# Kernel optimization log

Hardware: AMD Instinct MI355X
Metric: run time of the kernel (lower is better)

The kernel has to match this reference:

```python
import jax, jax.numpy as jnp
import numpy as np

N, E, B = 20000, 200000, 16
ND, ED, GD, HD, DOF = 64, 32, 32, 128, 6
PI = 3.14159265358979

def _hat(v):
    x, y, z = v[..., 0], v[..., 1], v[..., 2]
    O = jnp.zeros_like(x)
    return jnp.stack([jnp.stack([O, -z, y], -1),
                      jnp.stack([z, O, -x], -1),
                      jnp.stack([-y, x, O], -1)], -2)

def _so3_exp(phi):
    th2 = jnp.sum(phi * phi, -1, keepdims=True)
    th = jnp.sqrt(th2 + 1e-12)
    a = jnp.where(th < 1e-4, 1.0 - th2 / 6.0, jnp.sin(th) / th)
    b = jnp.where(th < 1e-4, 0.5 - th2 / 24.0, (1.0 - jnp.cos(th)) / th2)
    K = _hat(phi)
    I = jnp.eye(3, dtype=phi.dtype)
    return I + a[..., None] * K + b[..., None] * (K @ K)

def _se3_exp(rho, phi):
    # returns (R, t) of Exp([rho, phi]) with rotation part phi
    th2 = jnp.sum(phi * phi, -1, keepdims=True)
    th = jnp.sqrt(th2 + 1e-12)
    a = jnp.where(th < 1e-4, 1.0 - th2 / 6.0, jnp.sin(th) / th)
    b = jnp.where(th < 1e-4, 0.5 - th2 / 24.0, (1.0 - jnp.cos(th)) / th2)
    c = jnp.where(th < 1e-4, 1.0 / 6.0 - th2 / 120.0, (th - jnp.sin(th)) / (th2 * th))
    K = _hat(phi)
    KK = K @ K
    I = jnp.eye(3, dtype=phi.dtype)
    R = I + a[..., None] * K + b[..., None] * KK
    V = I + b[..., None] * K + c[..., None] * KK
    t = jnp.einsum('nij,nj->ni', V, rho)
    return R, t

def _comp(Ra, ta, Rb, tb):
    return Ra @ Rb, jnp.einsum('nij,nj->ni', Ra, tb) + ta

def _inv(R, t):
    Rt = jnp.swapaxes(R, -1, -2)
    return Rt, -jnp.einsum('nij,nj->ni', Rt, t)

def _vec(R, t):
    # flattened [R | t] 3x4 -> 12
    return jnp.concatenate([R, t[..., None]], -1).reshape(R.shape[0], 12)

def setup_inputs() -> dict:
    key = jax.random.key(0)
    ks = jax.random.split(key, 16)
    T_R = _so3_exp(0.5 * jax.random.normal(ks[0], (N, 3)))
    Tij_R = _so3_exp(0.5 * jax.random.normal(ks[1], (E, 3)))
    return {
        'xfeat': jax.random.normal(ks[2], (N, ND), jnp.float32),
        'T_R': T_R.astype(jnp.float32),
        'T_t': jax.random.normal(ks[3], (N, 3), jnp.float32),
        'edge_feat': jax.random.normal(ks[4], (E, ED), jnp.float32),
        'Tij_R': Tij_R.astype(jnp.float32),
        'Tij_t': jax.random.normal(ks[5], (E, 3), jnp.float32),
        'u': jax.random.normal(ks[6], (B, GD), jnp.float32),
        'edge_index': jax.random.randint(ks[7], (2, E), 0, N),
        'batch': jnp.sort(jax.random.randint(ks[8], (N,), 0, B)),
        'W1': 0.05 * jax.random.normal(ks[9], (2 * ND + 12 + ED, HD), jnp.float32),
        'b1': jnp.zeros((HD,), jnp.float32),
        'W2': 0.05 * jax.random.normal(ks[10], (HD, HD), jnp.float32),
        'b2': jnp.zeros((HD,), jnp.float32),
        'W3': 0.05 * jax.random.normal(ks[11], (HD + GD + ND, HD), jnp.float32),
        'b3': jnp.zeros((HD,), jnp.float32),
        'W4': 0.05 * jax.random.normal(ks[12], (HD, ND + DOF), jnp.float32),
        'b4': jnp.zeros((ND + DOF,), jnp.float32),
    }

def reference(xfeat, T_R, T_t, edge_feat, Tij_R, Tij_t, u,
              edge_index, batch, W1, b1, W2, b2, W3, b3, W4, b4):
    n = xfeat.shape[0]
    i, j = edge_index[0], edge_index[1]
    xfi, xfj = xfeat[i], xfeat[j]
    Ri, ti = T_R[i], T_t[i]
    Rj, tj = T_R[j], T_t[j]
    # T_err_ij = Tj * Ti.inv() * Tij_hat.inv()
    Rii, tii = _inv(Ri, ti)
    Ra, ta = _comp(Rj, tj, Rii, tii)
    Rhi, thi = _inv(Tij_R, Tij_t)
    Reij, teij = _comp(Ra, ta, Rhi, thi)
    # T_err_ji = Ti * Tj.inv() * Tij_hat
    Rji_, tji_ = _inv(Rj, tj)
    Rb, tb = _comp(Ri, ti, Rji_, tji_)
    Reji, teji = _comp(Rb, tb, Tij_R, Tij_t)
    f_ij = jnp.concatenate([xfi, xfj, edge_feat, _vec(Reij, teij)], 1)
    f_ji = jnp.concatenate([xfj, xfi, edge_feat, _vec(Reji, teji)], 1)
    feats = jnp.concatenate([f_ij, f_ji], 0)          # [2E, 172]
    j_both = jnp.concatenate([j, i], 0)               # [2E]
    h = jax.nn.relu(feats @ W1 + b1)
    h = jax.nn.relu(h @ W2 + b2)                      # [2E, HD]
    sums = jax.ops.segment_sum(h, j_both, num_segments=n)
    cnt = jax.ops.segment_sum(jnp.ones((h.shape[0], 1), h.dtype), j_both, num_segments=n)
    aggr = sums / jnp.maximum(cnt, 1.0)               # scatter_mean
    g = jnp.concatenate([aggr, xfeat, u[batch]], 1)
    out = jax.nn.relu(g @ W3 + b3) @ W4 + b4
    xupd, tupd = out[:, :-DOF], out[:, -DOF:]
    rho, phi = tupd[:, :3], tupd[:, 3:]
    # SquashRot: bound rotation angle to pi via tanh
    th = jnp.linalg.norm(phi, axis=-1, keepdims=True)
    phi = phi * (PI * jnp.tanh(th / PI) / (th + 1e-8))
    Rd, td = _se3_exp(rho, phi)
    R_out, t_out = _comp(Rd, td, T_R, T_t)            # boxplus_left: Exp(d) * T
    xfeat_out = xfeat + xupd
    theta = jnp.linalg.norm(phi, axis=-1, keepdims=True)
    return jnp.concatenate([xfeat_out, R_out.reshape(n, 9), t_out, theta], -1)
```

## Files before the change

kernel.cpp:

```cpp
#include <hip/hip_runtime.h>
#include <math.h>

#define ND 64
#define ED 32
#define GD 32
#define HD 128
#define DOF 6
#define K1 172
#define K1PAD 192
#define KG 224
#define N4P 80
#define NOUT 70
#define OUTC 77
#define MT 128
#define HP1 136
#define TDN 16
#define GP 232
#define HP 136
#define OP 84
#define MAXD 96
#define PI_F 3.14159265358979f

typedef short short8 __attribute__((ext_vector_type(8)));
typedef float f32x4  __attribute__((ext_vector_type(4)));

__device__ __forceinline__ unsigned short f2b(float f) {
    unsigned int u = __float_as_uint(f);
    u += 0x7fffu + ((u >> 16) & 1u);
    return (unsigned short)(u >> 16);
}
__device__ __forceinline__ float b2f(unsigned short b) {
    return __uint_as_float(((unsigned int)b) << 16);
}
__device__ __forceinline__ void mul33_abt(const float* A, const float* B, float* C) {
#pragma unroll
    for (int r = 0; r < 3; r++)
#pragma unroll
        for (int c = 0; c < 3; c++)
            C[3*r+c] = A[3*r+0]*B[3*c+0] + A[3*r+1]*B[3*c+1] + A[3*r+2]*B[3*c+2];
}

__global__ void __launch_bounds__(256)
prep(const float* __restrict__ W1, const float* __restrict__ W2,
     const float* __restrict__ W3, const float* __restrict__ W4,
     const float* __restrict__ xfeat, const float* __restrict__ edge_feat,
     unsigned short* __restrict__ W1b, unsigned short* __restrict__ W2b,
     unsigned short* __restrict__ W3b, unsigned short* __restrict__ W4b,
     unsigned short* __restrict__ xb, unsigned short* __restrict__ eb,
     int N, int E)
{
    int idx = blockIdx.x * 256 + threadIdx.x;
    if (idx < K1PAD * HD) {
        int k = idx >> 7, n = idx & 127;
        float v = (k < K1) ? W1[k * HD + n] : 0.f;
        int kc = k >> 5, kr = k & 31, q = kr >> 3, j = kr & 7;
        W1b[(((kc * 8 + (n >> 4)) * 4 + q) * 16 + (n & 15)) * 8 + j] = f2b(v);
        return;
    }
    idx -= K1PAD * HD;
    if (idx < HD * HD) {
        int k = idx >> 7, n = idx & 127;
        int kc = k >> 5, kr = k & 31, q = kr >> 3, j = kr & 7;
        W2b[(((kc * 8 + (n >> 4)) * 4 + q) * 16 + (n & 15)) * 8 + j] = f2b(W2[k * HD + n]);
        return;
    }
    idx -= HD * HD;
    if (idx < KG * HD) {
        int k = idx >> 7, n = idx & 127;
        int sk = (k < HD) ? ((k & 7) * 16 + (k >> 3)) : k;
        int kc = k >> 5, kr = k & 31, q = kr >> 3, j = kr & 7;
        W3b[(((kc * 8 + (n >> 4)) * 4 + q) * 16 + (n & 15)) * 8 + j] = f2b(W3[sk * HD + n]);
        return;
    }
    idx -= KG * HD;
    if (idx < HD * N4P) {
        int k = idx / N4P, n = idx % N4P;
        float v = (n < NOUT) ? W4[k * NOUT + n] : 0.f;
        int kc = k >> 5, kr = k & 31, q = kr >> 3, j = kr & 7;
        W4b[(((kc * 5 + (n >> 4)) * 4 + q) * 16 + (n & 15)) * 8 + j] = f2b(v);
        return;
    }
    idx -= HD * N4P;
    const int nx4 = N * ND / 4;
    if (idx < nx4) {
        const float4 v = *(const float4*)&xfeat[idx * 4];
        ushort4 o; o.x = f2b(v.x); o.y = f2b(v.y); o.z = f2b(v.z); o.w = f2b(v.w);
        *(ushort4*)&xb[idx * 4] = o;
        return;
    }
    idx -= nx4;
    if (idx < E * ED / 4) {
        const float4 v = *(const float4*)&edge_feat[idx * 4];
        ushort4 o; o.x = f2b(v.x); o.y = f2b(v.y); o.z = f2b(v.z); o.w = f2b(v.w);
        *(ushort4*)&eb[idx * 4] = o;
    }
}

__global__ void __launch_bounds__(256)
pose_csr(const float* __restrict__ T_R, const float* __restrict__ T_t,
         const float* __restrict__ Tij_R, const float* __restrict__ Tij_t,
         const int* __restrict__ edge_index,
         unsigned short* __restrict__ poseb, int* __restrict__ cnti,
         int* __restrict__ list, int E)
{
    const int g = blockIdx.x * 256 + threadIdx.x;
    if (g >= 2 * E) return;
    const bool fwd = (g < E);
    const int e = fwd ? g : g - E;
    const int ni = edge_index[e];
    const int nj = edge_index[E + e];
    const int tgt = fwd ? nj : ni;
    const int slot = atomicAdd(&cnti[tgt], 1);
    if (slot < MAXD) list[(size_t)tgt * MAXD + slot] = g;

    float Ri[9], Rj[9], TR[9], ti[3], tj[3], Tt[3];
#pragma unroll
    for (int q = 0; q < 9; q++) { Ri[q] = T_R[9*ni+q]; Rj[q] = T_R[9*nj+q]; TR[q] = Tij_R[9*e+q]; }
#pragma unroll
    for (int q = 0; q < 3; q++) { ti[q] = T_t[3*ni+q]; tj[q] = T_t[3*nj+q]; Tt[q] = Tij_t[3*e+q]; }
    float A[9];
    mul33_abt(Rj, Ri, A);
    float Re[9], te[3];
    if (fwd) {
        mul33_abt(A, TR, Re);
#pragma unroll
        for (int r = 0; r < 3; r++)
            te[r] = tj[r]
                  - (A[3*r+0]*ti[0] + A[3*r+1]*ti[1] + A[3*r+2]*ti[2])
                  - (Re[3*r+0]*Tt[0] + Re[3*r+1]*Tt[1] + Re[3*r+2]*Tt[2]);
    } else {
#pragma unroll
        for (int r = 0; r < 3; r++)
#pragma unroll
            for (int c = 0; c < 3; c++)
                Re[3*r+c] = A[r]*TR[c] + A[3+r]*TR[3+c] + A[6+r]*TR[6+c];
        const float d0 = Tt[0]-tj[0], d1 = Tt[1]-tj[1], d2 = Tt[2]-tj[2];
#pragma unroll
        for (int r = 0; r < 3; r++)
            te[r] = ti[r] + A[r]*d0 + A[3+r]*d1 + A[6+r]*d2;
    }
    short8 p0, p1;
#pragma unroll
    for (int r = 0; r < 2; r++) {
        p0[4*r+0] = (short)f2b(Re[3*r+0]);
        p0[4*r+1] = (short)f2b(Re[3*r+1]);
        p0[4*r+2] = (short)f2b(Re[3*r+2]);
        p0[4*r+3] = (short)f2b(te[r]);
    }
    p1[0] = (short)f2b(Re[6]); p1[1] = (short)f2b(Re[7]);
    p1[2] = (short)f2b(Re[8]); p1[3] = (short)f2b(te[2]);
    p1[4] = 0; p1[5] = 0; p1[6] = 0; p1[7] = 0;
    *(short8*)(poseb + (size_t)g * 16) = p0;
    *(short8*)(poseb + (size_t)g * 16 + 8) = p1;
}

__global__ void __launch_bounds__(256, 3)
edge_kernel(const unsigned short* __restrict__ xb, const unsigned short* __restrict__ eb,
            const unsigned short* __restrict__ poseb, const int* __restrict__ edge_index,
            const unsigned short* __restrict__ W1b, const float* __restrict__ b1,
            const unsigned short* __restrict__ W2b, const float* __restrict__ b2,
            unsigned short* __restrict__ hbuf, int E)
{
    __shared__ unsigned short h1s[4 * 32 * HP1];
    const int tid = threadIdx.x;
    const int wv = tid >> 6, lane = tid & 63;
    const int nl = lane & 15, quad = lane >> 4;
    const int D0 = blockIdx.x * MT + wv * 32;
    const int laneoff = quad * 128 + nl * 8;
    unsigned short* hw = h1s + wv * 32 * HP1;

    int s1[2], s2[2], ee[2], gg[2];
#pragma unroll
    for (int rt = 0; rt < 2; rt++) {
        int g = D0 + rt * 16 + nl;
        if (g >= 2 * E) g = 2 * E - 1;
        const bool fwd = (g < E);
        const int e = fwd ? g : g - E;
        const int ni = edge_index[e];
        const int nj = edge_index[E + e];
        s1[rt] = fwd ? ni : nj;
        s2[rt] = fwd ? nj : ni;
        ee[rt] = e; gg[rt] = g;
    }

    short8 a[2][6];
#pragma unroll
    for (int rt = 0; rt < 2; rt++) {
        a[rt][0] = *(const short8*)(xb + (size_t)s1[rt] * ND + quad * 8);
        a[rt][1] = *(const short8*)(xb + (size_t)s1[rt] * ND + 32 + quad * 8);
        a[rt][2] = *(const short8*)(xb + (size_t)s2[rt] * ND + quad * 8);
        a[rt][3] = *(const short8*)(xb + (size_t)s2[rt] * ND + 32 + quad * 8);
        a[rt][4] = *(const short8*)(eb + (size_t)ee[rt] * ED + quad * 8);
        a[rt][5] = (quad < 2) ? *(const short8*)(poseb + (size_t)gg[rt] * 16 + quad * 8)
                              : (short8)(short)0;
    }

    float bias1[8], bias2[8];
#pragma unroll
    for (int nt = 0; nt < 8; nt++) { bias1[nt] = b1[nt*16 + nl]; bias2[nt] = b2[nt*16 + nl]; }

    f32x4 acc[2][8];
#pragma unroll
    for (int rt = 0; rt < 2; rt++)
#pragma unroll
        for (int nt = 0; nt < 8; nt++) acc[rt][nt] = (f32x4)0.f;

#pragma unroll
    for (int kc = 0; kc < 6; kc++) {
#pragma unroll
        for (int nt = 0; nt < 8; nt++) {
            short8 b = *(const short8*)(W1b + (kc*8 + nt)*512 + laneoff);
            acc[0][nt] = __builtin_amdgcn_mfma_f32_16x16x32_bf16(a[0][kc], b, acc[0][nt], 0, 0, 0);
            acc[1][nt] = __builtin_amdgcn_mfma_f32_16x16x32_bf16(a[1][kc], b, acc[1][nt], 0, 0, 0);
        }
    }

#pragma unroll
    for (int rt = 0; rt < 2; rt++)
#pragma unroll
        for (int nt = 0; nt < 8; nt++) {
            const int col = nt*16 + nl;
#pragma unroll
            for (int r = 0; r < 4; r++)
                hw[(rt*16 + quad*4 + r) * HP1 + col] = f2b(fmaxf(acc[rt][nt][r] + bias1[nt], 0.f));
        }
    asm volatile("s_waitcnt lgkmcnt(0)" ::: "memory");

#pragma unroll
    for (int rt = 0; rt < 2; rt++)
#pragma unroll
        for (int nt = 0; nt < 8; nt++) acc[rt][nt] = (f32x4)0.f;
#pragma unroll
    for (int kc = 0; kc < 4; kc++) {
        short8 a0 = *(const short8*)&hw[( 0 + nl) * HP1 + kc*32 + quad*8];
        short8 a1 = *(const short8*)&hw[(16 + nl) * HP1 + kc*32 + quad*8];
#pragma unroll
        for (int nt = 0; nt < 8; nt++) {
            short8 b = *(const short8*)(W2b + (kc*8 + nt)*512 + laneoff);
            acc[0][nt] = __builtin_amdgcn_mfma_f32_16x16x32_bf16(a0, b, acc[0][nt], 0, 0, 0);
            acc[1][nt] = __builtin_amdgcn_mfma_f32_16x16x32_bf16(a1, b, acc[1][nt], 0, 0, 0);
        }
    }

#pragma unroll
    for (int rt = 0; rt < 2; rt++)
#pragma unroll
        for (int r = 0; r < 4; r++) {
            const int g2 = D0 + rt*16 + quad*4 + r;
            if (g2 < 2 * E) {
                short8 hv;
#pragma unroll
                for (int nt = 0; nt < 8; nt++)
                    hv[nt] = (short)f2b(fmaxf(acc[rt][nt][r] + bias2[nt], 0.f));
                *(short8*)(hbuf + (size_t)g2 * HD + nl*8) = hv;
            }
        }
}

__global__ void __launch_bounds__(256)
node_kernel(const float* __restrict__ xfeat, const float* __restrict__ T_R,
            const float* __restrict__ T_t, const float* __restrict__ u,
            const int* __restrict__ batch,
            const unsigned short* __restrict__ W3b, const float* __restrict__ b3,
            const unsigned short* __restrict__ W4b, const float* __restrict__ b4,
            const unsigned short* __restrict__ hbuf, const int* __restrict__ list,
            const int* __restrict__ cnti,
            float* __restrict__ out, int Nn)
{
    __shared__ unsigned short gbuf[TDN * GP];
    __shared__ unsigned short hid[TDN * HP];
    __shared__ float obuf[TDN * OP];
    const int tid = threadIdx.x;
    const int wv = tid >> 6, lane = tid & 63;
    const int n0 = blockIdx.x * TDN;
    const int nn = min(TDN, Nn - n0);

#pragma unroll
    for (int i = 0; i < 4; i++) {
        const int d = wv + 4*i;
        if (d < nn) {
            const int n = n0 + d;
            const int deg = cnti[n];
            const int degl = min(deg, MAXD);
            const float inv = 1.0f / (float)max(deg, 1);
            const int* lp = list + (size_t)n * MAXD;
            float a0 = 0.f, a1 = 0.f;
            int k = 0;
            for (; k + 2 <= degl; k += 2) {
                const int e0 = lp[k], e1 = lp[k+1];
                const unsigned int v0 = *(const unsigned int*)(hbuf + (size_t)e0 * HD + 2*lane);
                const unsigned int v1 = *(const unsigned int*)(hbuf + (size_t)e1 * HD + 2*lane);
                a0 += b2f((unsigned short)v0) + b2f((unsigned short)v1);
                a1 += b2f((unsigned short)(v0 >> 16)) + b2f((unsigned short)(v1 >> 16));
            }
            if (k < degl) {
                const unsigned int v0 = *(const unsigned int*)(hbuf + (size_t)lp[k] * HD + 2*lane);
                a0 += b2f((unsigned short)v0);
                a1 += b2f((unsigned short)(v0 >> 16));
            }
            const unsigned int pk = (unsigned int)f2b(a0 * inv) | ((unsigned int)f2b(a1 * inv) << 16);
            *(unsigned int*)&gbuf[d * GP + 2*lane] = pk;
        }
    }
    for (int idx = tid; idx < TDN * 24; idx += 256) {
        const int d = idx / 24;
        if (d < nn) {
            const int n = n0 + d;
            const int c4 = (idx % 24) * 4;
            float4 v;
            if (c4 < 64) v = *(const float4*)&xfeat[(size_t)n * ND + c4];
            else         v = *(const float4*)&u[(size_t)batch[n] * GD + (c4 - 64)];
            ushort4 o; o.x = f2b(v.x); o.y = f2b(v.y); o.z = f2b(v.z); o.w = f2b(v.w);
            *(ushort4*)&gbuf[d * GP + 128 + c4] = o;
        }
    }
    __syncthreads();

    const int nl = lane & 15, quad = lane >> 4;
    const int laneoff = quad * 128 + nl * 8;

    f32x4 acc3[2];
    acc3[0] = (f32x4)0.f; acc3[1] = (f32x4)0.f;
#pragma unroll
    for (int kc = 0; kc < 7; kc++) {
        short8 A0 = *(const short8*)&gbuf[nl * GP + kc*32 + quad*8];
#pragma unroll
        for (int t = 0; t < 2; t++) {
            short8 B = *(const short8*)(W3b + (kc*8 + wv*2 + t)*512 + laneoff);
            acc3[t] = __builtin_amdgcn_mfma_f32_16x16x32_bf16(A0, B, acc3[t], 0, 0, 0);
        }
    }
#pragma unroll
    for (int t = 0; t < 2; t++) {
        const int col = (wv*2 + t)*16 + nl;
        const float bb = b3[col];
#pragma unroll
        for (int r = 0; r < 4; r++)
            hid[(quad*4 + r) * HP + col] = f2b(fmaxf(acc3[t][r] + bb, 0.f));
    }
    __syncthreads();

    f32x4 acc4[2];
    acc4[0] = (f32x4)0.f; acc4[1] = (f32x4)0.f;
    const int nt1 = (wv == 0) ? 4 : -1;
#pragma unroll
    for (int kc = 0; kc < 4; kc++) {
        short8 A0 = *(const short8*)&hid[nl * HP + kc*32 + quad*8];
        short8 B0 = *(const short8*)(W4b + (kc*5 + wv)*512 + laneoff);
        acc4[0] = __builtin_amdgcn_mfma_f32_16x16x32_bf16(A0, B0, acc4[0], 0, 0, 0);
        if (nt1 >= 0) {
            short8 B1 = *(const short8*)(W4b + (kc*5 + nt1)*512 + laneoff);
            acc4[1] = __builtin_amdgcn_mfma_f32_16x16x32_bf16(A0, B1, acc4[1], 0, 0, 0);
        }
    }
    {
        const int col0 = wv*16 + nl;
        const float bb0 = (col0 < NOUT) ? b4[col0] : 0.f;
#pragma unroll
        for (int r = 0; r < 4; r++)
            obuf[(quad*4 + r) * OP + col0] = acc4[0][r] + bb0;
        if (nt1 >= 0) {
            const int col1 = nt1*16 + nl;
            const float bb1 = (col1 < NOUT) ? b4[col1] : 0.f;
#pragma unroll
            for (int r = 0; r < 4; r++)
                obuf[(quad*4 + r) * OP + col1] = acc4[1][r] + bb1;
        }
    }
    __syncthreads();

    for (int idx = tid; idx < TDN * ND; idx += 256) {
        const int d = idx >> 6, c = idx & 63;
        if (d < nn) {
            const int n = n0 + d;
            out[(size_t)n * OUTC + c] = xfeat[(size_t)n * ND + c] + obuf[d * OP + c];
        }
    }
    if (tid < nn) {
        const int n = n0 + tid;
        const float r0 = obuf[tid*OP + 64], r1 = obuf[tid*OP + 65], r2 = obuf[tid*OP + 66];
        float p0 = obuf[tid*OP + 67], p1 = obuf[tid*OP + 68], p2 = obuf[tid*OP + 69];
        const float th0 = sqrtf(p0*p0 + p1*p1 + p2*p2);
        const float s = PI_F * tanhf(th0 / PI_F) / (th0 + 1e-8f);
        p0 *= s; p1 *= s; p2 *= s;
        const float pp = p0*p0 + p1*p1 + p2*p2;
        const float th = sqrtf(pp + 1e-12f);
        float a, b, c;
        if (th < 1e-4f) { a = 1.f - pp/6.f; b = 0.5f - pp/24.f; c = 1.f/6.f - pp/120.f; }
        else { const float sn = sinf(th), cs = cosf(th); a = sn/th; b = (1.f-cs)/pp; c = (th-sn)/(pp*th); }
        float Rd[9], V[9];
        Rd[0]=1.f+b*(p0*p0-pp); Rd[1]=-a*p2+b*p0*p1; Rd[2]= a*p1+b*p0*p2;
        Rd[3]= a*p2+b*p1*p0;    Rd[4]=1.f+b*(p1*p1-pp); Rd[5]=-a*p0+b*p1*p2;
        Rd[6]=-a*p1+b*p2*p0;    Rd[7]= a*p0+b*p2*p1;  Rd[8]=1.f+b*(p2*p2-pp);
        V[0]=1.f+c*(p0*p0-pp);  V[1]=-b*p2+c*p0*p1;   V[2]= b*p1+c*p0*p2;
        V[3]= b*p2+c*p1*p0;     V[4]=1.f+c*(p1*p1-pp); V[5]=-b*p0+c*p1*p2;
        V[6]=-b*p1+c*p2*p0;     V[7]= b*p0+c*p2*p1;   V[8]=1.f+c*(p2*p2-pp);
        const float td0 = V[0]*r0 + V[1]*r1 + V[2]*r2;
        const float td1 = V[3]*r0 + V[4]*r1 + V[5]*r2;
        const float td2 = V[6]*r0 + V[7]*r1 + V[8]*r2;
        float TRn[9], Ttn[3];
#pragma unroll
        for (int q = 0; q < 9; q++) TRn[q] = T_R[9*n+q];
#pragma unroll
        for (int q = 0; q < 3; q++) Ttn[q] = T_t[3*n+q];
        float* o = out + (size_t)n * OUTC + 64;
#pragma unroll
        for (int r = 0; r < 3; r++)
#pragma unroll
            for (int cc = 0; cc < 3; cc++)
                o[3*r+cc] = Rd[3*r+0]*TRn[cc] + Rd[3*r+1]*TRn[3+cc] + Rd[3*r+2]*TRn[6+cc];
        o[9]  = Rd[0]*Ttn[0] + Rd[1]*Ttn[1] + Rd[2]*Ttn[2] + td0;
        o[10] = Rd[3]*Ttn[0] + Rd[4]*Ttn[1] + Rd[5]*Ttn[2] + td1;
        o[11] = Rd[6]*Ttn[0] + Rd[7]*Ttn[1] + Rd[8]*Ttn[2] + td2;
        o[12] = sqrtf(pp);
    }
}

extern "C" void kernel_launch(void* const* d_in, const int* in_sizes, int n_in,
                              void* d_out, int out_size, void* d_ws, size_t ws_size,
                              hipStream_t stream)
{
    const float* xfeat     = (const float*)d_in[0];
    const float* T_R       = (const float*)d_in[1];
    const float* T_t       = (const float*)d_in[2];
    const float* edge_feat = (const float*)d_in[3];
    const float* Tij_R     = (const float*)d_in[4];
    const float* Tij_t     = (const float*)d_in[5];
    const float* u         = (const float*)d_in[6];
    const int*   edge_index= (const int*)d_in[7];
    const int*   batch     = (const int*)d_in[8];
    const float* W1 = (const float*)d_in[9],  *b1 = (const float*)d_in[10];
    const float* W2 = (const float*)d_in[11], *b2 = (const float*)d_in[12];
    const float* W3 = (const float*)d_in[13], *b3 = (const float*)d_in[14];
    const float* W4 = (const float*)d_in[15], *b4 = (const float*)d_in[16];
    const int N = in_sizes[0] / ND;
    const int E = in_sizes[3] / ED;

    char* p = (char*)d_ws;
    unsigned short* W1b = (unsigned short*)p;   p += (size_t)K1PAD * HD * 2;
    unsigned short* W2b = (unsigned short*)p;   p += (size_t)HD * HD * 2;
    unsigned short* W3b = (unsigned short*)p;   p += (size_t)KG * HD * 2;
    unsigned short* W4b = (unsigned short*)p;   p += (size_t)HD * N4P * 2;
    unsigned short* xb  = (unsigned short*)p;   p += (size_t)N * ND * 2;
    unsigned short* ebf = (unsigned short*)p;   p += (size_t)E * ED * 2;
    unsigned short* poseb = (unsigned short*)p; p += (size_t)2 * E * 16 * 2;
    unsigned short* hbuf = (unsigned short*)p;  p += (size_t)2 * E * HD * 2;
    int* list = (int*)p;                        p += (size_t)N * MAXD * 4;
    int* cnti = (int*)p;

    hipMemsetAsync(cnti, 0, (size_t)N * 4, stream);
    const int prepn = K1PAD*HD + HD*HD + KG*HD + HD*N4P + N*ND/4 + E*ED/4;
    prep<<<(prepn + 255) / 256, 256, 0, stream>>>(W1, W2, W3, W4, xfeat, edge_feat,
                                                  W1b, W2b, W3b, W4b, xb, ebf, N, E);
    pose_csr<<<(2*E + 255) / 256, 256, 0, stream>>>(T_R, T_t, Tij_R, Tij_t, edge_index,
                                                    poseb, cnti, list, E);
    const int ebk = (2 * E + MT - 1) / MT;
    edge_kernel<<<ebk, 256, 0, stream>>>(xb, ebf, poseb, edge_index,
                                         W1b, b1, W2b, b2, hbuf, E);
    const int nb = (N + TDN - 1) / TDN;
    node_kernel<<<nb, 256, 0, stream>>>(xfeat, T_R, T_t, u, batch, W3b, b3, W4b, b4,
                                        hbuf, list, cnti, (float*)d_out, N);
}
```

Before: 295.8 us.

## Swap MFMA operands to transposed layout and double-buffer weight loads in edge MLP

```diff
diff --git a/kernel.cpp b/kernel.cpp
--- a/kernel.cpp
+++ b/kernel.cpp
@@ -13,7 +13,7 @@
 #define NOUT 70
 #define OUTC 77
 #define MT 128
-#define HP1 136
+#define P1 132
 #define TDN 16
 #define GP 232
 #define HP 136
@@ -67,9 +67,8 @@
     idx -= HD * HD;
     if (idx < KG * HD) {
         int k = idx >> 7, n = idx & 127;
-        int sk = (k < HD) ? ((k & 7) * 16 + (k >> 3)) : k;
         int kc = k >> 5, kr = k & 31, q = kr >> 3, j = kr & 7;
-        W3b[(((kc * 8 + (n >> 4)) * 4 + q) * 16 + (n & 15)) * 8 + j] = f2b(W3[sk * HD + n]);
+        W3b[(((kc * 8 + (n >> 4)) * 4 + q) * 16 + (n & 15)) * 8 + j] = f2b(W3[k * HD + n]);
         return;
     }
     idx -= KG * HD;
@@ -161,13 +160,13 @@
             const unsigned short* __restrict__ W2b, const float* __restrict__ b2,
             unsigned short* __restrict__ hbuf, int E)
 {
-    __shared__ unsigned short h1s[4 * 32 * HP1];
+    __shared__ unsigned short h1s[4 * 32 * P1];
     const int tid = threadIdx.x;
     const int wv = tid >> 6, lane = tid & 63;
     const int nl = lane & 15, quad = lane >> 4;
     const int D0 = blockIdx.x * MT + wv * 32;
     const int laneoff = quad * 128 + nl * 8;
-    unsigned short* hw = h1s + wv * 32 * HP1;
+    unsigned short* hw = h1s + wv * 32 * P1;
 
     int s1[2], s2[2], ee[2], gg[2];
 #pragma unroll
@@ -195,66 +194,91 @@
                               : (short8)(short)0;
     }
 
-    float bias1[8], bias2[8];
-#pragma unroll
-    for (int nt = 0; nt < 8; nt++) { bias1[nt] = b1[nt*16 + nl]; bias2[nt] = b2[nt*16 + nl]; }
-
     f32x4 acc[2][8];
 #pragma unroll
     for (int rt = 0; rt < 2; rt++)
 #pragma unroll
-        for (int nt = 0; nt < 8; nt++) acc[rt][nt] = (f32x4)0.f;
-
+        for (int At = 0; At < 8; At++) acc[rt][At] = (f32x4)0.f;
+    short8 wbuf[2][8];
+#pragma unroll
+    for (int At = 0; At < 8; At++)
+        wbuf[0][At] = *(const short8*)(W1b + At * 512 + laneoff);
 #pragma unroll
     for (int kc = 0; kc < 6; kc++) {
-#pragma unroll
-        for (int nt = 0; nt < 8; nt++) {
-            short8 b = *(const short8*)(W1b + (kc*8 + nt)*512 + laneoff);
-            acc[0][nt] = __builtin_amdgcn_mfma_f32_16x16x32_bf16(a[0][kc], b, acc[0][nt], 0, 0, 0);
-            acc[1][nt] = __builtin_amdgcn_mfma_f32_16x16x32_bf16(a[1][kc], b, acc[1][nt], 0, 0, 0);
-        }
-    }
-
+        const int cur = kc & 1, nxt = cur ^ 1;
+        if (kc < 5) {
+#pragma unroll
+            for (int At = 0; At < 8; At++)
+                wbuf[nxt][At] = *(const short8*)(W1b + ((kc + 1) * 8 + At) * 512 + laneoff);
+        }
+#pragma unroll
+        for (int At = 0; At < 8; At++) {
+            acc[0][At] = __builtin_amdgcn_mfma_f32_16x16x32_bf16(wbuf[cur][At], a[0][kc], acc[0][At], 0, 0, 0);
+            acc[1][At] = __builtin_amdgcn_mfma_f32_16x16x32_bf16(wbuf[cur][At], a[1][kc], acc[1][At], 0, 0, 0);
+        }
+    }
+
+#pragma unroll
+    for (int At = 0; At < 8; At++) {
+        const f32x4 bv = *(const f32x4*)&b1[At * 16 + quad * 4];
+#pragma unroll
+        for (int rt = 0; rt < 2; rt++) {
+            unsigned int lo = (unsigned int)f2b(fmaxf(acc[rt][At][0] + bv[0], 0.f))
+                            | ((unsigned int)f2b(fmaxf(acc[rt][At][1] + bv[1], 0.f)) << 16);
+            unsigned int hi = (unsigned int)f2b(fmaxf(acc[rt][At][2] + bv[2], 0.f))
+                            | ((unsigned int)f2b(fmaxf(acc[rt][At][3] + bv[3], 0.f)) << 16);
+            uint2 pk; pk.x = lo; pk.y = hi;
+            *(uint2*)&hw[(rt * 16 + nl) * P1 + At * 16 + quad * 4] = pk;
+        }
+    }
+    asm volatile("s_waitcnt lgkmcnt(0)" ::: "memory");
+
+    f32x4 acc2[2][8];
 #pragma unroll
     for (int rt = 0; rt < 2; rt++)
 #pragma unroll
-        for (int nt = 0; nt < 8; nt++) {
-            const int col = nt*16 + nl;
-#pragma unroll
-            for (int r = 0; r < 4; r++)
-                hw[(rt*16 + quad*4 + r) * HP1 + col] = f2b(fmaxf(acc[rt][nt][r] + bias1[nt], 0.f));
-        }
-    asm volatile("s_waitcnt lgkmcnt(0)" ::: "memory");
-
-#pragma unroll
-    for (int rt = 0; rt < 2; rt++)
-#pragma unroll
-        for (int nt = 0; nt < 8; nt++) acc[rt][nt] = (f32x4)0.f;
+        for (int At = 0; At < 8; At++) acc2[rt][At] = (f32x4)0.f;
+#pragma unroll
+    for (int At = 0; At < 8; At++)
+        wbuf[0][At] = *(const short8*)(W2b + At * 512 + laneoff);
 #pragma unroll
     for (int kc = 0; kc < 4; kc++) {
-        short8 a0 = *(const short8*)&hw[( 0 + nl) * HP1 + kc*32 + quad*8];
-        short8 a1 = *(const short8*)&hw[(16 + nl) * HP1 + kc*32 + quad*8];
-#pragma unroll
-        for (int nt = 0; nt < 8; nt++) {
-            short8 b = *(const short8*)(W2b + (kc*8 + nt)*512 + laneoff);
-            acc[0][nt] = __builtin_amdgcn_mfma_f32_16x16x32_bf16(a0, b, acc[0][nt], 0, 0, 0);
-            acc[1][nt] = __builtin_amdgcn_mfma_f32_16x16x32_bf16(a1, b, acc[1][nt], 0, 0, 0);
-        }
-    }
-
-#pragma unroll
-    for (int rt = 0; rt < 2; rt++)
-#pragma unroll
-        for (int r = 0; r < 4; r++) {
-            const int g2 = D0 + rt*16 + quad*4 + r;
+        union { short8 s; uint2 u[2]; } hv[2];
+#pragma unroll
+        for (int rt = 0; rt < 2; rt++) {
+            const unsigned short* hp = &hw[(rt * 16 + nl) * P1 + kc * 32 + quad * 8];
+            hv[rt].u[0] = *(const uint2*)hp;
+            hv[rt].u[1] = *(const uint2*)(hp + 4);
+        }
+        const int cur = kc & 1, nxt = cur ^ 1;
+        if (kc < 3) {
+#pragma unroll
+            for (int At = 0; At < 8; At++)
+                wbuf[nxt][At] = *(const short8*)(W2b + ((kc + 1) * 8 + At) * 512 + laneoff);
+        }
+#pragma unroll
+        for (int At = 0; At < 8; At++) {
+            acc2[0][At] = __builtin_amdgcn_mfma_f32_16x16x32_bf16(wbuf[cur][At], hv[0].s, acc2[0][At], 0, 0, 0);
+            acc2[1][At] = __builtin_amdgcn_mfma_f32_16x16x32_bf16(wbuf[cur][At], hv[1].s, acc2[1][At], 0, 0, 0);
+        }
+    }
+
+#pragma unroll
+    for (int At = 0; At < 8; At++) {
+        const f32x4 bv = *(const f32x4*)&b2[At * 16 + quad * 4];
+#pragma unroll
+        for (int rt = 0; rt < 2; rt++) {
+            const int g2 = D0 + rt * 16 + nl;
             if (g2 < 2 * E) {
-                short8 hv;
-#pragma unroll
-                for (int nt = 0; nt < 8; nt++)
-                    hv[nt] = (short)f2b(fmaxf(acc[rt][nt][r] + bias2[nt], 0.f));
-                *(short8*)(hbuf + (size_t)g2 * HD + nl*8) = hv;
+                unsigned int lo = (unsigned int)f2b(fmaxf(acc2[rt][At][0] + bv[0], 0.f))
+                                | ((unsigned int)f2b(fmaxf(acc2[rt][At][1] + bv[1], 0.f)) << 16);
+                unsigned int hi = (unsigned int)f2b(fmaxf(acc2[rt][At][2] + bv[2], 0.f))
+                                | ((unsigned int)f2b(fmaxf(acc2[rt][At][3] + bv[3], 0.f)) << 16);
+                uint2 pk; pk.x = lo; pk.y = hi;
+                *(uint2*)(hbuf + (size_t)g2 * HD + At * 16 + quad * 4) = pk;
             }
         }
+    }
 }
 
 __global__ void __launch_bounds__(256)
```

Measured after the change: 304.2 us. 2.8% more time.

## Sort edge directions by target node via CSR and enlarge edge MLP tile

Applied to the files above, without the earlier changes.

```diff
diff --git a/kernel.cpp b/kernel.cpp
--- a/kernel.cpp
+++ b/kernel.cpp
@@ -12,13 +12,12 @@
 #define N4P 80
 #define NOUT 70
 #define OUTC 77
-#define MT 128
-#define HP1 136
+#define MT 256
+#define P1 144
 #define TDN 16
 #define GP 232
 #define HP 136
 #define OP 84
-#define MAXD 96
 #define PI_F 3.14159265358979f
 
 typedef short short8 __attribute__((ext_vector_type(8)));
@@ -97,22 +96,63 @@
 }
 
 __global__ void __launch_bounds__(256)
-pose_csr(const float* __restrict__ T_R, const float* __restrict__ T_t,
-         const float* __restrict__ Tij_R, const float* __restrict__ Tij_t,
-         const int* __restrict__ edge_index,
-         unsigned short* __restrict__ poseb, int* __restrict__ cnti,
-         int* __restrict__ list, int E)
-{
-    const int g = blockIdx.x * 256 + threadIdx.x;
+count_kernel(const int* __restrict__ edge_index, int* __restrict__ cnti, int E)
+{
+    int g = blockIdx.x * 256 + threadIdx.x;
     if (g >= 2 * E) return;
-    const bool fwd = (g < E);
-    const int e = fwd ? g : g - E;
+    const int tgt = (g < E) ? edge_index[E + g] : edge_index[g - E];
+    atomicAdd(&cnti[tgt], 1);
+}
+
+__global__ void __launch_bounds__(1024)
+scan_kernel(const int* __restrict__ cnti, int* __restrict__ off,
+            int* __restrict__ cursor, int N)
+{
+    __shared__ int part[1024];
+    const int t = threadIdx.x;
+    const int chunk = (N + 1023) / 1024;
+    const int base = t * chunk;
+    int s = 0;
+    for (int i = 0; i < chunk; i++) { int idx = base + i; if (idx < N) s += cnti[idx]; }
+    part[t] = s;
+    __syncthreads();
+    for (int d = 1; d < 1024; d <<= 1) {
+        int v = (t >= d) ? part[t - d] : 0;
+        __syncthreads();
+        part[t] += v;
+        __syncthreads();
+    }
+    int pre = (t > 0) ? part[t - 1] : 0;
+    for (int i = 0; i < chunk; i++) {
+        int idx = base + i;
+        if (idx < N) { off[idx] = pre; cursor[idx] = pre; pre += cnti[idx]; }
+    }
+}
+
+__global__ void __launch_bounds__(256)
+scatter_kernel(const int* __restrict__ edge_index, int* __restrict__ cursor,
+               int* __restrict__ dlist, int E)
+{
+    int g = blockIdx.x * 256 + threadIdx.x;
+    if (g >= 2 * E) return;
+    const int tgt = (g < E) ? edge_index[E + g] : edge_index[g - E];
+    const int pos = atomicAdd(&cursor[tgt], 1);
+    dlist[pos] = g;
+}
+
+__global__ void __launch_bounds__(256)
+pose_kernel(const float* __restrict__ T_R, const float* __restrict__ T_t,
+            const float* __restrict__ Tij_R, const float* __restrict__ Tij_t,
+            const int* __restrict__ edge_index, const int* __restrict__ dlist,
+            unsigned short* __restrict__ poseb, int E)
+{
+    const int p = blockIdx.x * 256 + threadIdx.x;
+    if (p >= 2 * E) return;
+    const int dir = dlist[p];
+    const bool fwd = (dir < E);
+    const int e = fwd ? dir : dir - E;
     const int ni = edge_index[e];
     const int nj = edge_index[E + e];
-    const int tgt = fwd ? nj : ni;
-    const int slot = atomicAdd(&cnti[tgt], 1);
-    if (slot < MAXD) list[(size_t)tgt * MAXD + slot] = g;
-
     float Ri[9], Rj[9], TR[9], ti[3], tj[3], Tt[3];
 #pragma unroll
     for (int q = 0; q < 9; q++) { Ri[q] = T_R[9*ni+q]; Rj[q] = T_R[9*nj+q]; TR[q] = Tij_R[9*e+q]; }
@@ -150,111 +190,142 @@
     p1[0] = (short)f2b(Re[6]); p1[1] = (short)f2b(Re[7]);
     p1[2] = (short)f2b(Re[8]); p1[3] = (short)f2b(te[2]);
     p1[4] = 0; p1[5] = 0; p1[6] = 0; p1[7] = 0;
-    *(short8*)(poseb + (size_t)g * 16) = p0;
-    *(short8*)(poseb + (size_t)g * 16 + 8) = p1;
-}
-
-__global__ void __launch_bounds__(256, 3)
+    *(short8*)(poseb + (size_t)p * 16) = p0;
+    *(short8*)(poseb + (size_t)p * 16 + 8) = p1;
+}
+
+__global__ void __launch_bounds__(256, 2)
 edge_kernel(const unsigned short* __restrict__ xb, const unsigned short* __restrict__ eb,
             const unsigned short* __restrict__ poseb, const int* __restrict__ edge_index,
+            const int* __restrict__ dlist,
             const unsigned short* __restrict__ W1b, const float* __restrict__ b1,
             const unsigned short* __restrict__ W2b, const float* __restrict__ b2,
             unsigned short* __restrict__ hbuf, int E)
 {
-    __shared__ unsigned short h1s[4 * 32 * HP1];
+    __shared__ unsigned short h1s[4 * 64 * P1];
     const int tid = threadIdx.x;
     const int wv = tid >> 6, lane = tid & 63;
     const int nl = lane & 15, quad = lane >> 4;
-    const int D0 = blockIdx.x * MT + wv * 32;
+    const int D0 = blockIdx.x * MT + wv * 64;
     const int laneoff = quad * 128 + nl * 8;
-    unsigned short* hw = h1s + wv * 32 * HP1;
-
-    int s1[2], s2[2], ee[2], gg[2];
-#pragma unroll
-    for (int rt = 0; rt < 2; rt++) {
-        int g = D0 + rt * 16 + nl;
-        if (g >= 2 * E) g = 2 * E - 1;
-        const bool fwd = (g < E);
-        const int e = fwd ? g : g - E;
+    const int twoE = 2 * E;
+    unsigned short* hw = h1s + wv * 64 * P1;
+
+    int s1[4], s2[4], ee[4], pp[4];
+#pragma unroll
+    for (int rt = 0; rt < 4; rt++) {
+        int p = D0 + rt * 16 + nl;
+        if (p >= twoE) p = twoE - 1;
+        pp[rt] = p;
+        const int dir = dlist[p];
+        const bool fwd = (dir < E);
+        const int e = fwd ? dir : dir - E;
         const int ni = edge_index[e];
         const int nj = edge_index[E + e];
         s1[rt] = fwd ? ni : nj;
         s2[rt] = fwd ? nj : ni;
-        ee[rt] = e; gg[rt] = g;
-    }
-
-    short8 a[2][6];
-#pragma unroll
-    for (int rt = 0; rt < 2; rt++) {
-        a[rt][0] = *(const short8*)(xb + (size_t)s1[rt] * ND + quad * 8);
-        a[rt][1] = *(const short8*)(xb + (size_t)s1[rt] * ND + 32 + quad * 8);
-        a[rt][2] = *(const short8*)(xb + (size_t)s2[rt] * ND + quad * 8);
-        a[rt][3] = *(const short8*)(xb + (size_t)s2[rt] * ND + 32 + quad * 8);
-        a[rt][4] = *(const short8*)(eb + (size_t)ee[rt] * ED + quad * 8);
-        a[rt][5] = (quad < 2) ? *(const short8*)(poseb + (size_t)gg[rt] * 16 + quad * 8)
-                              : (short8)(short)0;
-    }
-
-    float bias1[8], bias2[8];
-#pragma unroll
-    for (int nt = 0; nt < 8; nt++) { bias1[nt] = b1[nt*16 + nl]; bias2[nt] = b2[nt*16 + nl]; }
-
-    f32x4 acc[2][8];
-#pragma unroll
-    for (int rt = 0; rt < 2; rt++)
+        ee[rt] = e;
+    }
+
+    f32x4 acc[4][8];
+#pragma unroll
+    for (int rt = 0; rt < 4; rt++)
 #pragma unroll
         for (int nt = 0; nt < 8; nt++) acc[rt][nt] = (f32x4)0.f;
 
+    short8 wf[2][8];
+#pragma unroll
+    for (int nt = 0; nt < 8; nt++)
+        wf[0][nt] = *(const short8*)(W1b + nt * 512 + laneoff);
+
 #pragma unroll
     for (int kc = 0; kc < 6; kc++) {
-#pragma unroll
-        for (int nt = 0; nt < 8; nt++) {
-            short8 b = *(const short8*)(W1b + (kc*8 + nt)*512 + laneoff);
-            acc[0][nt] = __builtin_amdgcn_mfma_f32_16x16x32_bf16(a[0][kc], b, acc[0][nt], 0, 0, 0);
-            acc[1][nt] = __builtin_amdgcn_mfma_f32_16x16x32_bf16(a[1][kc], b, acc[1][nt], 0, 0, 0);
-        }
-    }
-
-#pragma unroll
-    for (int rt = 0; rt < 2; rt++)
-#pragma unroll
-        for (int nt = 0; nt < 8; nt++) {
-            const int col = nt*16 + nl;
-#pragma unroll
-            for (int r = 0; r < 4; r++)
-                hw[(rt*16 + quad*4 + r) * HP1 + col] = f2b(fmaxf(acc[rt][nt][r] + bias1[nt], 0.f));
-        }
+        short8 af[4];
+#pragma unroll
+        for (int rt = 0; rt < 4; rt++) {
+            switch (kc) {
+            case 0: af[rt] = *(const short8*)(xb + (size_t)s1[rt] * ND + quad * 8); break;
+            case 1: af[rt] = *(const short8*)(xb + (size_t)s1[rt] * ND + 32 + quad * 8); break;
+            case 2: af[rt] = *(const short8*)(xb + (size_t)s2[rt] * ND + quad * 8); break;
+            case 3: af[rt] = *(const short8*)(xb + (size_t)s2[rt] * ND + 32 + quad * 8); break;
+            case 4: af[rt] = *(const short8*)(eb + (size_t)ee[rt] * ED + quad * 8); break;
+            default: af[rt] = (quad < 2) ? *(const short8*)(poseb + (size_t)pp[rt] * 16 + quad * 8)
+                                         : (short8)(short)0; break;
+            }
+        }
+        const int cur = kc & 1, nxt = cur ^ 1;
+        if (kc < 5) {
+#pragma unroll
+            for (int nt = 0; nt < 8; nt++)
+                wf[nxt][nt] = *(const short8*)(W1b + ((kc + 1) * 8 + nt) * 512 + laneoff);
+        }
+#pragma unroll
+        for (int nt = 0; nt < 8; nt++)
+#pragma unroll
+            for (int rt = 0; rt < 4; rt++)
+                acc[rt][nt] = __builtin_amdgcn_mfma_f32_16x16x32_bf16(af[rt], wf[cur][nt], acc[rt][nt], 0, 0, 0);
+    }
+
+    {
+        float bias1[8];
+#pragma unroll
+        for (int nt = 0; nt < 8; nt++) bias1[nt] = b1[nt * 16 + nl];
+#pragma unroll
+        for (int rt = 0; rt < 4; rt++)
+#pragma unroll
+            for (int nt = 0; nt < 8; nt++) {
+                const int col = nt * 16 + nl;
+#pragma unroll
+                for (int r = 0; r < 4; r++)
+                    hw[(rt * 16 + quad * 4 + r) * P1 + col] = f2b(fmaxf(acc[rt][nt][r] + bias1[nt], 0.f));
+            }
+    }
     asm volatile("s_waitcnt lgkmcnt(0)" ::: "memory");
 
 #pragma unroll
-    for (int rt = 0; rt < 2; rt++)
+    for (int rt = 0; rt < 4; rt++)
 #pragma unroll
         for (int nt = 0; nt < 8; nt++) acc[rt][nt] = (f32x4)0.f;
 #pragma unroll
+    for (int nt = 0; nt < 8; nt++)
+        wf[0][nt] = *(const short8*)(W2b + nt * 512 + laneoff);
+#pragma unroll
     for (int kc = 0; kc < 4; kc++) {
-        short8 a0 = *(const short8*)&hw[( 0 + nl) * HP1 + kc*32 + quad*8];
-        short8 a1 = *(const short8*)&hw[(16 + nl) * HP1 + kc*32 + quad*8];
-#pragma unroll
-        for (int nt = 0; nt < 8; nt++) {
-            short8 b = *(const short8*)(W2b + (kc*8 + nt)*512 + laneoff);
-            acc[0][nt] = __builtin_amdgcn_mfma_f32_16x16x32_bf16(a0, b, acc[0][nt], 0, 0, 0);
-            acc[1][nt] = __builtin_amdgcn_mfma_f32_16x16x32_bf16(a1, b, acc[1][nt], 0, 0, 0);
-        }
-    }
-
-#pragma unroll
-    for (int rt = 0; rt < 2; rt++)
-#pragma unroll
-        for (int r = 0; r < 4; r++) {
-            const int g2 = D0 + rt*16 + quad*4 + r;
-            if (g2 < 2 * E) {
-                short8 hv;
-#pragma unroll
-                for (int nt = 0; nt < 8; nt++)
-                    hv[nt] = (short)f2b(fmaxf(acc[rt][nt][r] + bias2[nt], 0.f));
-                *(short8*)(hbuf + (size_t)g2 * HD + nl*8) = hv;
+        short8 hf[4];
+#pragma unroll
+        for (int rt = 0; rt < 4; rt++)
+            hf[rt] = *(const short8*)&hw[(rt * 16 + nl) * P1 + kc * 32 + quad * 8];
+        const int cur = kc & 1, nxt = cur ^ 1;
+        if (kc < 3) {
+#pragma unroll
+            for (int nt = 0; nt < 8; nt++)
+                wf[nxt][nt] = *(const short8*)(W2b + ((kc + 1) * 8 + nt) * 512 + laneoff);
+        }
+#pragma unroll
+        for (int nt = 0; nt < 8; nt++)
+#pragma unroll
+            for (int rt = 0; rt < 4; rt++)
+                acc[rt][nt] = __builtin_amdgcn_mfma_f32_16x16x32_bf16(hf[rt], wf[cur][nt], acc[rt][nt], 0, 0, 0);
+    }
+
+    {
+        float bias2[8];
+#pragma unroll
+        for (int nt = 0; nt < 8; nt++) bias2[nt] = b2[nt * 16 + nl];
+#pragma unroll
+        for (int rt = 0; rt < 4; rt++)
+#pragma unroll
+            for (int r = 0; r < 4; r++) {
+                const int p2 = D0 + rt * 16 + quad * 4 + r;
+                if (p2 < twoE) {
+                    short8 hv;
+#pragma unroll
+                    for (int nt = 0; nt < 8; nt++)
+                        hv[nt] = (short)f2b(fmaxf(acc[rt][nt][r] + bias2[nt], 0.f));
+                    *(short8*)(hbuf + (size_t)p2 * HD + nl * 8) = hv;
+                }
             }
-        }
+    }
 }
 
 __global__ void __launch_bounds__(256)
@@ -263,7 +334,7 @@
             const int* __restrict__ batch,
             const unsigned short* __restrict__ W3b, const float* __restrict__ b3,
             const unsigned short* __restrict__ W4b, const float* __restrict__ b4,
-            const unsigned short* __restrict__ hbuf, const int* __restrict__ list,
+            const unsigned short* __restrict__ hbuf, const int* __restrict__ off,
             const int* __restrict__ cnti,
             float* __restrict__ out, int Nn)
 {
@@ -277,29 +348,34 @@
 
 #pragma unroll
     for (int i = 0; i < 4; i++) {
-        const int d = wv + 4*i;
+        const int d = wv + 4 * i;
         if (d < nn) {
             const int n = n0 + d;
             const int deg = cnti[n];
-            const int degl = min(deg, MAXD);
+            const int start = off[n];
             const float inv = 1.0f / (float)max(deg, 1);
-            const int* lp = list + (size_t)n * MAXD;
+            const unsigned short* hp = hbuf + (size_t)start * HD + 2 * lane;
             float a0 = 0.f, a1 = 0.f;
             int k = 0;
-            for (; k + 2 <= degl; k += 2) {
-                const int e0 = lp[k], e1 = lp[k+1];
-                const unsigned int v0 = *(const unsigned int*)(hbuf + (size_t)e0 * HD + 2*lane);
-                const unsigned int v1 = *(const unsigned int*)(hbuf + (size_t)e1 * HD + 2*lane);
-                a0 += b2f((unsigned short)v0) + b2f((unsigned short)v1);
-                a1 += b2f((unsigned short)(v0 >> 16)) + b2f((unsigned short)(v1 >> 16));
+            for (; k + 4 <= deg; k += 4) {
+                const unsigned int v0 = *(const unsigned int*)(hp);
+                const unsigned int v1 = *(const unsigned int*)(hp + HD);
+                const unsigned int v2 = *(const unsigned int*)(hp + 2 * HD);
+                const unsigned int v3 = *(const unsigned int*)(hp + 3 * HD);
+                hp += 4 * HD;
+                a0 += b2f((unsigned short)v0) + b2f((unsigned short)v1)
+                    + b2f((unsigned short)v2) + b2f((unsigned short)v3);
+                a1 += b2f((unsigned short)(v0 >> 16)) + b2f((unsigned short)(v1 >> 16))
+                    + b2f((unsigned short)(v2 >> 16)) + b2f((unsigned short)(v3 >> 16));
             }
-            if (k < degl) {
-                const unsigned int v0 = *(const unsigned int*)(hbuf + (size_t)lp[k] * HD + 2*lane);
+            for (; k < deg; k++) {
+                const unsigned int v0 = *(const unsigned int*)(hp);
+                hp += HD;
                 a0 += b2f((unsigned short)v0);
                 a1 += b2f((unsigned short)(v0 >> 16));
             }
             const unsigned int pk = (unsigned int)f2b(a0 * inv) | ((unsigned int)f2b(a1 * inv) << 16);
-            *(unsigned int*)&gbuf[d * GP + 2*lane] = pk;
+            *(unsigned int*)&gbuf[d * GP + 2 * lane] = pk;
         }
     }
     for (int idx = tid; idx < TDN * 24; idx += 256) {
@@ -323,20 +399,20 @@
     acc3[0] = (f32x4)0.f; acc3[1] = (f32x4)0.f;
 #pragma unroll
     for (int kc = 0; kc < 7; kc++) {
-        short8 A0 = *(const short8*)&gbuf[nl * GP + kc*32 + quad*8];
+        short8 A0 = *(const short8*)&gbuf[nl * GP + kc * 32 + quad * 8];
 #pragma unroll
         for (int t = 0; t < 2; t++) {
-            short8 B = *(const short8*)(W3b + (kc*8 + wv*2 + t)*512 + laneoff);
+            short8 B = *(const short8*)(W3b + (kc * 8 + wv * 2 + t) * 512 + laneoff);
             acc3[t] = __builtin_amdgcn_mfma_f32_16x16x32_bf16(A0, B, acc3[t], 0, 0, 0);
         }
     }
 #pragma unroll
     for (int t = 0; t < 2; t++) {
-        const int col = (wv*2 + t)*16 + nl;
+        const int col = (wv * 2 + t) * 16 + nl;
         const float bb = b3[col];
 #pragma unroll
         for (int r = 0; r < 4; r++)
-            hid[(quad*4 + r) * HP + col] = f2b(fmaxf(acc3[t][r] + bb, 0.f));
+            hid[(quad * 4 + r) * HP + col] = f2b(fmaxf(acc3[t][r] + bb, 0.f));
     }
     __syncthreads();
 
@@ -345,26 +421,26 @@
     const int nt1 = (wv == 0) ? 4 : -1;
 #pragma unroll
     for (int kc = 0; kc < 4; kc++) {
-        short8 A0 = *(const short8*)&hid[nl * HP + kc*32 + quad*8];
-        short8 B0 = *(const short8*)(W4b + (kc*5 + wv)*512 + laneoff);
+        short8 A0 = *(const short8*)&hid[nl * HP + kc * 32 + quad * 8];
+        short8 B0 = *(const short8*)(W4b + (kc * 5 + wv) * 512 + laneoff);
         acc4[0] = __builtin_amdgcn_mfma_f32_16x16x32_bf16(A0, B0, acc4[0], 0, 0, 0);
         if (nt1 >= 0) {
-            short8 B1 = *(const short8*)(W4b + (kc*5 + nt1)*512 + laneoff);
+            short8 B1 = *(const short8*)(W4b + (kc * 5 + nt1) * 512 + laneoff);
             acc4[1] = __builtin_amdgcn_mfma_f32_16x16x32_bf16(A0, B1, acc4[1], 0, 0, 0);
         }
     }
     {
-        const int col0 = wv*16 + nl;
+        const int col0 = wv * 16 + nl;
         const float bb0 = (col0 < NOUT) ? b4[col0] : 0.f;
 #pragma unroll
         for (int r = 0; r < 4; r++)
-            obuf[(quad*4 + r) * OP + col0] = acc4[0][r] + bb0;
+            obuf[(quad * 4 + r) * OP + col0] = acc4[0][r] + bb0;
         if (nt1 >= 0) {
-            const int col1 = nt1*16 + nl;
+            const int col1 = nt1 * 16 + nl;
             const float bb1 = (col1 < NOUT) ? b4[col1] : 0.f;
 #pragma unroll
             for (int r = 0; r < 4; r++)
-                obuf[(quad*4 + r) * OP + col1] = acc4[1][r] + bb1;
+                obuf[(quad * 4 + r) * OP + col1] = acc4[1][r] + bb1;
         }
     }
     __syncthreads();
@@ -445,19 +521,24 @@
     unsigned short* ebf = (unsigned short*)p;   p += (size_t)E * ED * 2;
     unsigned short* poseb = (unsigned short*)p; p += (size_t)2 * E * 16 * 2;
     unsigned short* hbuf = (unsigned short*)p;  p += (size_t)2 * E * HD * 2;
-    int* list = (int*)p;                        p += (size_t)N * MAXD * 4;
-    int* cnti = (int*)p;
+    int* dlist = (int*)p;                       p += (size_t)2 * E * 4;
+    int* cnti = (int*)p;                        p += (size_t)N * 4;
+    int* off  = (int*)p;                        p += (size_t)N * 4;
+    int* cursor = (int*)p;
 
     hipMemsetAsync(cnti, 0, (size_t)N * 4, stream);
     const int prepn = K1PAD*HD + HD*HD + KG*HD + HD*N4P + N*ND/4 + E*ED/4;
     prep<<<(prepn + 255) / 256, 256, 0, stream>>>(W1, W2, W3, W4, xfeat, edge_feat,
                                                   W1b, W2b, W3b, W4b, xb, ebf, N, E);
-    pose_csr<<<(2*E + 255) / 256, 256, 0, stream>>>(T_R, T_t, Tij_R, Tij_t, edge_index,
-                                                    poseb, cnti, list, E);
+    count_kernel<<<(2*E + 255) / 256, 256, 0, stream>>>(edge_index, cnti, E);
+    scan_kernel<<<1, 1024, 0, stream>>>(cnti, off, cursor, N);
+    scatter_kernel<<<(2*E + 255) / 256, 256, 0, stream>>>(edge_index, cursor, dlist, E);
+    pose_kernel<<<(2*E + 255) / 256, 256, 0, stream>>>(T_R, T_t, Tij_R, Tij_t,
+                                                       edge_index, dlist, poseb, E);
     const int ebk = (2 * E + MT - 1) / MT;
-    edge_kernel<<<ebk, 256, 0, stream>>>(xb, ebf, poseb, edge_index,
+    edge_kernel<<<ebk, 256, 0, stream>>>(xb, ebf, poseb, edge_index, dlist,
                                          W1b, b1, W2b, b2, hbuf, E);
     const int nb = (N + TDN - 1) / TDN;
     node_kernel<<<nb, 256, 0, stream>>>(xfeat, T_R, T_t, u, batch, W3b, b3, W4b, b4,
-                                        hbuf, list, cnti, (float*)d_out, N);
-}
+                                        hbuf, off, cnti, (float*)d_out, N);
+}
```

Measured after the change: 324.2 us. 1.1x slower.
